# Kernel tuning notes

Hardware: AMD Instinct MI355X
Metric: run time of the kernel (lower is better)

Reference implementation:

```python
import jax, jax.numpy as jnp
import numpy as np

B, T, H, OUT, L = 125, 512, 512, 1024, 2


def _rnn_layer(xs, w_ih, w_hh, b_ih, b_hh):
    # xs: [B, T, H_in] -> scan over time with tanh recurrence
    xs_t = jnp.swapaxes(xs, 0, 1)  # [T, B, H_in]
    h0 = jnp.zeros((xs.shape[0], w_hh.shape[0]), dtype=xs.dtype)

    def step(h, x_t):
        h = jnp.tanh(x_t @ w_ih.T + b_ih + h @ w_hh.T + b_hh)
        return h, h

    h_last, hs = jax.lax.scan(step, h0, xs_t)
    return jnp.swapaxes(hs, 0, 1), h_last  # [B, T, H], [B, H]


def setup_inputs() -> dict:
    key = jax.random.key(0)
    ks = jax.random.split(key, 8)
    s = 1.0 / np.sqrt(H)
    x = jax.random.normal(ks[0], (B, T, H), dtype=jnp.float32)
    w_ih = jax.random.uniform(ks[1], (L, H, H), jnp.float32, -s, s)
    w_hh = jax.random.uniform(ks[2], (L, H, H), jnp.float32, -s, s)
    b_ih = jax.random.uniform(ks[3], (L, H), jnp.float32, -s, s)
    b_hh = jax.random.uniform(ks[4], (L, H), jnp.float32, -s, s)
    fc_w = jax.random.uniform(ks[5], (OUT, H), jnp.float32, -s, s)
    fc_b = jax.random.uniform(ks[6], (OUT,), jnp.float32, -s, s)
    return {"x": x, "w_ih": w_ih, "w_hh": w_hh, "b_ih": b_ih,
            "b_hh": b_hh, "fc_w": fc_w, "fc_b": fc_b}


def reference(x, w_ih, w_hh, b_ih, b_hh, fc_w, fc_b):
    h = x
    finals = []
    for l in range(L):  # small fixed layer loop
        h, h_last = _rnn_layer(h, w_ih[l], w_hh[l], b_ih[l], b_hh[l])
        finals.append(h_last)
    hidden = jnp.stack(finals, axis=0)  # [L, B, H]
    out = h.reshape(-1, H) @ fc_w.T + fc_b  # [B*T, OUT]
    return out, hidden
```

## Files before the change

kernel.cpp:

```cpp
#include <hip/hip_runtime.h>
#include <hip/hip_bf16.h>
#include <cstdint>

typedef short short8 __attribute__((ext_vector_type(8)));
typedef float f32x4 __attribute__((ext_vector_type(4)));
typedef uint32_t u32x2 __attribute__((ext_vector_type(2)));
typedef unsigned short u16;

#define DEVINL __device__ __forceinline__

DEVINL u16 f32_to_bf16(float f) {
  uint32_t u = __builtin_bit_cast(uint32_t, f);
  u += 0x7FFFu + ((u >> 16) & 1u);
  return (u16)(u >> 16);
}
DEVINL float bf16_to_f32(u16 b) {
  return __builtin_bit_cast(float, ((uint32_t)b) << 16);
}
DEVINL f32x4 mfma16(short8 a, short8 b, f32x4 c) {
  return __builtin_amdgcn_mfma_f32_16x16x32_bf16(a, b, c, 0, 0, 0);
}
DEVINL float tanh_e2(float x) {
  float e = __builtin_amdgcn_exp2f(x * 2.88539008177793f);
  return 1.f - __fdividef(2.f, 1.f + e);
}
DEVINL uint32_t cvt_pk_bf16(float lo, float hi) {
  uint32_t r;
  asm("v_cvt_pk_bf16_f32 %0, %1, %2" : "=v"(r) : "v"(lo), "v"(hi));
  return r;
}

__global__ void conv_bf16(const float* __restrict__ src, u16* __restrict__ dst, long n) {
  long i = ((long)blockIdx.x * blockDim.x + threadIdx.x) * 4;
  long stride = (long)gridDim.x * blockDim.x * 4;
  for (; i < n; i += stride) {
    float4 v = *(const float4*)(src + i);
    uint64_t p = (uint64_t)f32_to_bf16(v.x)
               | ((uint64_t)f32_to_bf16(v.y) << 16)
               | ((uint64_t)f32_to_bf16(v.z) << 32)
               | ((uint64_t)f32_to_bf16(v.w) << 48);
    *(uint64_t*)(dst + i) = p;
  }
}

__global__ void prep_bias(const float* __restrict__ bih, const float* __restrict__ bhh,
                          float* __restrict__ b1, float* __restrict__ b2) {
  int i = threadIdx.x;
  b1[i] = bih[i]       + bhh[i];
  b2[i] = bih[512 + i] + bhh[512 + i];
}

DEVINL void rec_window(char* LDS, int g, const u16* __restrict__ Whh,
                       const u16* __restrict__ U, u16* __restrict__ Hout,
                       float* __restrict__ hidden, u16* __restrict__ hstate, int win) {
  const int tid  = threadIdx.x;
  const int lane = tid & 63;
  const int w    = tid >> 6;
  const int q    = lane >> 4;
  const int r16  = lane & 15;
  const int t0   = win << 7;

  short8 wreg[3][16];
#pragma unroll
  for (int tt = 0; tt < 3; ++tt)
#pragma unroll
    for (int kk = 0; kk < 16; ++kk)
      wreg[tt][kk] = *(const short8*)(Whh + (size_t)(w * 64 + tt * 16 + r16) * 512 + kk * 32 + q * 8);

#pragma unroll
  for (int kk = 0; kk < 16; ++kk) {
    short8 v = *(const short8*)(Whh + (size_t)(w * 64 + 48 + r16) * 512 + kk * 32 + q * 8);
    *(short8*)(LDS + w * 16384 + kk * 1024 + q * 256 + r16 * 16) = v;
  }

  if (win == 0) {
    short8 z = {0, 0, 0, 0, 0, 0, 0, 0};
    *(short8*)(LDS + 131072 + tid * 32)      = z;
    *(short8*)(LDS + 131072 + tid * 32 + 16) = z;
  } else {
    short8 a = *(const short8*)(hstate + (size_t)g * 8192 + tid * 16);
    short8 b = *(const short8*)(hstate + (size_t)g * 8192 + tid * 16 + 8);
    *(short8*)(LDS + 131072 + tid * 32)      = a;
    *(short8*)(LDS + 131072 + tid * 32 + 16) = b;
  }

  uint32_t rd  = 131072 + q * 256 + r16 * 16;
  uint32_t wrb = 147456 + w * 2048 + (q >> 1) * 256 + r16 * 16 + (q & 1) * 8;
  const uint32_t wlb = w * 16384 + q * 256 + r16 * 16;
  const int jb = w * 64 + q * 4;
  const char* Ub = (const char*)U;
  const uint32_t ubase = (uint32_t)(g * 512 + tid) * 32;
  char* Hc = (char*)Hout;
  uint32_t hoff = (uint32_t)(g * 16 + r16) * 524288u + (uint32_t)jb * 2u + (uint32_t)t0 * 1024u;

  short8 u  = *(const short8*)(Ub + ubase + (uint32_t)t0 * 131072u);
  short8 u2 = *(const short8*)(Ub + ubase + (uint32_t)t0 * 131072u + 16);
  __syncthreads();

  for (int t = t0; t < t0 + 128; ++t) {
    f32x4 D0, D1, D2, D3;
#pragma unroll
    for (int rg = 0; rg < 4; ++rg) {
      D0[rg] = bf16_to_f32((u16)u[rg]);
      D1[rg] = bf16_to_f32((u16)u[rg + 4]);
      D2[rg] = bf16_to_f32((u16)u2[rg]);
      D3[rg] = bf16_to_f32((u16)u2[rg + 4]);
    }
    {
      uint32_t off = ubase + (uint32_t)((t + 1 <= 511) ? (t + 1) : 511) * 131072u;
      u  = *(const short8*)(Ub + off);
      u2 = *(const short8*)(Ub + off + 16);
    }
#pragma unroll
    for (int kk = 0; kk < 16; ++kk) {
      short8 hf = *(const short8*)(LDS + rd + kk * 1024);
      short8 wl = *(const short8*)(LDS + wlb + kk * 1024);
      D0 = mfma16(wreg[0][kk], hf, D0);
      D1 = mfma16(wreg[1][kk], hf, D1);
      D2 = mfma16(wreg[2][kk], hf, D2);
      D3 = mfma16(wl, hf, D3);
    }
#define EPI_TILE(Dt, tt) { \
    float e0 = tanh_e2(Dt[0]), e1 = tanh_e2(Dt[1]); \
    float e2 = tanh_e2(Dt[2]), e3 = tanh_e2(Dt[3]); \
    u32x2 pk; pk[0] = cvt_pk_bf16(e0, e1); pk[1] = cvt_pk_bf16(e2, e3); \
    *(u32x2*)(LDS + wrb + ((tt) >> 1) * 1024 + ((tt) & 1) * 512) = pk; \
    *(u32x2*)(Hc + hoff + (tt) * 32) = pk; \
  }
    EPI_TILE(D0, 0); EPI_TILE(D1, 1); EPI_TILE(D2, 2); EPI_TILE(D3, 3);
#undef EPI_TILE
    hoff += 1024;

    rd ^= 16384; wrb ^= 16384;
    asm volatile("s_waitcnt lgkmcnt(0)" ::: "memory");
    __builtin_amdgcn_s_barrier();
    asm volatile("" ::: "memory");
  }

  {
    short8 a = *(const short8*)(LDS + 131072 + tid * 32);
    short8 b = *(const short8*)(LDS + 131072 + tid * 32 + 16);
    *(short8*)(hstate + (size_t)g * 8192 + tid * 16)     = a;
    *(short8*)(hstate + (size_t)g * 8192 + tid * 16 + 8) = b;
  }

  if (win == 3) {
    int b = g * 16 + r16;
    if (b < 125) {
      uint32_t fwr = 131072 + w * 2048 + (q >> 1) * 256 + r16 * 16 + (q & 1) * 8;
#pragma unroll
      for (int tt = 0; tt < 4; ++tt) {
        u32x2 pk = *(const u32x2*)(LDS + fwr + (tt >> 1) * 1024 + (tt & 1) * 512);
        float4 v;
        v.x = __builtin_bit_cast(float, pk[0] << 16);
        v.y = __builtin_bit_cast(float, pk[0] & 0xFFFF0000u);
        v.z = __builtin_bit_cast(float, pk[1] << 16);
        v.w = __builtin_bit_cast(float, pk[1] & 0xFFFF0000u);
        *(float4*)(hidden + (size_t)b * 512 + jb + tt * 16) = v;
      }
    }
  }
}

DEVINL void gemm_tile(char* LDS, const u16* __restrict__ A, const u16* __restrict__ B,
                      const float* __restrict__ bias, void* __restrict__ out,
                      int brow, int bcol, int N, int frag) {
  u16* lA = (u16*)LDS;
  u16* lB = (u16*)(LDS + 16384);
  const int tid  = threadIdx.x;
  const int lane = tid & 63;
  const int wave = tid >> 6;
  const int wr = wave >> 2;
  const int wc = wave & 3;
  const int q   = lane >> 4;
  const int r16 = lane & 15;

  f32x4 acc[4][2];
#pragma unroll
  for (int i = 0; i < 4; ++i)
#pragma unroll
    for (int j = 0; j < 2; ++j) acc[i][j] = (f32x4){0.f, 0.f, 0.f, 0.f};

  for (int kt = 0; kt < 8; ++kt) {
#pragma unroll
    for (int s = 0; s < 2; ++s) {
      int c   = tid * 2 + s;
      int row = c >> 3;
      int cb  = (c & 7) * 16;
      int dsw = cb ^ ((row & 7) << 4);
      short8 va = *(const short8*)(A + (size_t)(brow + row) * 512 + kt * 64 + (cb >> 1));
      *(short8*)((char*)lA + row * 128 + dsw) = va;
      short8 vb = *(const short8*)(B + (size_t)(bcol + row) * 512 + kt * 64 + (cb >> 1));
      *(short8*)((char*)lB + row * 128 + dsw) = vb;
    }
    __syncthreads();
#pragma unroll
    for (int kk = 0; kk < 2; ++kk) {
      short8 af[4], bfr[2];
#pragma unroll
      for (int mt = 0; mt < 4; ++mt) {
        int row = wr * 64 + mt * 16 + r16;
        int byt = (kk * 64 + q * 16) ^ ((row & 7) << 4);
        af[mt] = *(const short8*)((const char*)lA + row * 128 + byt);
      }
#pragma unroll
      for (int nt = 0; nt < 2; ++nt) {
        int row = wc * 32 + nt * 16 + r16;
        int byt = (kk * 64 + q * 16) ^ ((row & 7) << 4);
        bfr[nt] = *(const short8*)((const char*)lB + row * 128 + byt);
      }
#pragma unroll
      for (int mt = 0; mt < 4; ++mt)
#pragma unroll
        for (int nt = 0; nt < 2; ++nt)
          acc[mt][nt] = mfma16(af[mt], bfr[nt], acc[mt][nt]);
    }
    __syncthreads();
  }

#pragma unroll
  for (int mt = 0; mt < 4; ++mt) {
#pragma unroll
    for (int nt = 0; nt < 2; ++nt) {
      int jc = bcol + wc * 32 + nt * 16 + r16;
      float bv = bias[jc];
      if (!frag) {
#pragma unroll
        for (int rg = 0; rg < 4; ++rg) {
          int mg = brow + wr * 64 + mt * 16 + q * 4 + rg;
          ((float*)out)[(size_t)mg * N + jc] = acc[mt][nt][rg] + bv;
        }
      } else {
        int tidc    = (jc >> 6) * 64 + ((jc >> 2) & 3) * 16;
        int colpart = ((jc >> 4) & 3) * 4 + (jc & 3);
#pragma unroll
        for (int rg = 0; rg < 4; ++rg) {
          int mg = brow + wr * 64 + mt * 16 + q * 4 + rg;
          int bb = mg >> 9;
          int t2 = mg & 511;
          size_t idx = (((size_t)t2 * 8 + (bb >> 4)) * 512 + tidc + (bb & 15)) * 16 + colpart;
          ((u16*)out)[idx] = f32_to_bf16(acc[mt][nt][rg] + bv);
        }
      }
    }
  }
}

__attribute__((amdgpu_flat_work_group_size(512, 512), amdgpu_waves_per_eu(2, 2)))
__global__ void phase(const u16* __restrict__ Whh1, const u16* __restrict__ Whh2,
                      u16* __restrict__ U1, u16* __restrict__ U2,
                      u16* __restrict__ H1, u16* __restrict__ H2,
                      u16* __restrict__ hs1, u16* __restrict__ hs2,
                      const u16* __restrict__ Xb, const u16* __restrict__ Wih1,
                      const u16* __restrict__ Wih2, const u16* __restrict__ FCW,
                      const float* __restrict__ b1, const float* __restrict__ b2,
                      const float* __restrict__ fcb,
                      float* __restrict__ outp, float* __restrict__ hid,
                      int rec1w, int rec2w, int njobs, int j0, int j1, int j2) {
  __shared__ char LDS[163840];
  const int bx = blockIdx.x;
  if (bx < 8) {
    if (rec1w >= 0) rec_window(LDS, bx, Whh1, U1, H1, hid, hs1, rec1w);
  } else if (bx < 16) {
    if (rec2w >= 0) rec_window(LDS, bx - 8, Whh2, U2, H2, hid + 64000, hs2, rec2w);
  } else if (njobs > 0) {
    const int widx = bx - 16;
    int jobs[3] = {j0, j1, j2};
    int cnt[3], total = 0;
    for (int i = 0; i < njobs; ++i) { cnt[i] = ((jobs[i] >> 2) == 2) ? 1000 : 500; total += cnt[i]; }
    for (int tile = widx; tile < total; tile += 240) {
      int rem = tile, jj = 0;
      while (jj < njobs - 1 && rem >= cnt[jj]) { rem -= cnt[jj]; ++jj; }
      int kind = jobs[jj] >> 2, wn = jobs[jj] & 3;
      if (kind == 0)
        gemm_tile(LDS, Xb, Wih1, b1, U1, (rem >> 2) * 512 + wn * 128, (rem & 3) * 128, 512, 1);
      else if (kind == 1)
        gemm_tile(LDS, H1, Wih2, b2, U2, (rem >> 2) * 512 + wn * 128, (rem & 3) * 128, 512, 1);
      else
        gemm_tile(LDS, H2, FCW, fcb, outp, (rem >> 3) * 512 + wn * 128, (rem & 7) * 128, 1024, 0);
    }
  }
}

#define J(k, w) ((k) * 4 + (w))

extern "C" void kernel_launch(void* const* d_in, const int* in_sizes, int n_in,
                              void* d_out, int out_size, void* d_ws, size_t ws_size,
                              hipStream_t stream) {
  const float* x   = (const float*)d_in[0];
  const float* wih = (const float*)d_in[1];
  const float* whh = (const float*)d_in[2];
  const float* bih = (const float*)d_in[3];
  const float* bhh = (const float*)d_in[4];
  const float* fcw = (const float*)d_in[5];
  const float* fcb = (const float*)d_in[6];

  char* ws = (char*)d_ws;
  float* outp = (float*)d_out;
  float* hid  = outp + 65536000;
  u16*   U1   = (u16*)d_out;

  u16* Wih1 = (u16*)(ws + 0);
  u16* Whh1 = (u16*)(ws + 524288);
  u16* Wih2 = (u16*)(ws + 1048576);
  u16* Whh2 = (u16*)(ws + 1572864);
  u16* FCW  = (u16*)(ws + 2097152);
  float* b1 = (float*)(ws + 3145728);
  float* b2 = b1 + 512;
  u16* hs1  = (u16*)(ws + 3276800);
  u16* hs2  = (u16*)(ws + 3407872);

  conv_bf16<<<2048, 256, 0, stream>>>(x, (u16*)(ws + 4194304), 32768000L);
  conv_bf16<<<256, 256, 0, stream>>>(wih,          Wih1, 262144L);
  conv_bf16<<<256, 256, 0, stream>>>(wih + 262144, Wih2, 262144L);
  conv_bf16<<<256, 256, 0, stream>>>(whh,          Whh1, 262144L);
  conv_bf16<<<256, 256, 0, stream>>>(whh + 262144, Whh2, 262144L);
  conv_bf16<<<512, 256, 0, stream>>>(fcw, FCW, 524288L);
  prep_bias<<<1, 512, 0, stream>>>(bih, bhh, b1, b2);

  u16* Xb = (u16*)(ws + 4194304);

  if (ws_size >= 205520896ull) {
    u16* U2 = (u16*)(ws + 4194304);
    u16* H1 = (u16*)(ws + 71303168);
    u16* H2 = (u16*)(ws + 138412032);
#define PH(r1, r2, nj, a, b, c) \
    phase<<<256, 512, 0, stream>>>(Whh1, Whh2, U1, U2, H1, H2, hs1, hs2, Xb, \
                                   Wih1, Wih2, FCW, b1, b2, fcb, outp, hid, \
                                   r1, r2, nj, a, b, c)
    PH(-1, -1, 1, J(0,0), 0, 0);
    PH( 0, -1, 3, J(0,1), J(0,2), J(0,3));
    PH( 1, -1, 1, J(1,0), 0, 0);
    PH( 2,  0, 1, J(1,1), 0, 0);
    PH( 3,  1, 1, J(1,2), 0, 0);
    PH(-1,  2, 2, J(1,3), J(2,0), 0);
    PH(-1,  3, 2, J(2,1), J(2,2), 0);
    PH(-1, -1, 1, J(2,3), 0, 0);
#undef PH
  } else {
    u16* U2 = U1;
    u16* H1 = (u16*)(ws + 70303744);
    u16* H2 = H1;
#define PH(r1, r2, nj, a, b, c) \
    phase<<<256, 512, 0, stream>>>(Whh1, Whh2, U1, U2, H1, H2, hs1, hs2, Xb, \
                                   Wih1, Wih2, FCW, b1, b2, fcb, outp, hid, \
                                   r1, r2, nj, a, b, c)
    PH(-1, -1, 3, J(0,0), J(0,1), J(0,2));
    PH(-1, -1, 1, J(0,3), 0, 0);
    PH( 0, -1, 0, 0, 0, 0);
    PH( 1, -1, 0, 0, 0, 0);
    PH( 2, -1, 0, 0, 0, 0);
    PH( 3, -1, 0, 0, 0, 0);
    PH(-1, -1, 3, J(1,0), J(1,1), J(1,2));
    PH(-1, -1, 1, J(1,3), 0, 0);
    PH(-1,  0, 0, 0, 0, 0);
    PH(-1,  1, 0, 0, 0, 0);
    PH(-1,  2, 0, 0, 0, 0);
    PH(-1,  3, 0, 0, 0, 0);
    PH(-1, -1, 2, J(2,0), J(2,1), 0);
    PH(-1, -1, 2, J(2,2), J(2,3), 0);
#undef PH
  }

  (void)in_sizes; (void)n_in; (void)out_size;
}
```

Before: 1.904 ms.

## Halve recurrence windows for finer overlap and fuse x conversion into GEMM

```diff
diff --git a/kernel.cpp b/kernel.cpp
--- a/kernel.cpp
+++ b/kernel.cpp
@@ -58,7 +58,7 @@
   const int w    = tid >> 6;
   const int q    = lane >> 4;
   const int r16  = lane & 15;
-  const int t0   = win << 7;
+  const int t0   = win << 6;
 
   short8 wreg[3][16];
 #pragma unroll
@@ -97,7 +97,7 @@
   short8 u2 = *(const short8*)(Ub + ubase + (uint32_t)t0 * 131072u + 16);
   __syncthreads();
 
-  for (int t = t0; t < t0 + 128; ++t) {
+  for (int t = t0; t < t0 + 64; ++t) {
     f32x4 D0, D1, D2, D3;
 #pragma unroll
     for (int rg = 0; rg < 4; ++rg) {
@@ -144,7 +144,7 @@
     *(short8*)(hstate + (size_t)g * 8192 + tid * 16 + 8) = b;
   }
 
-  if (win == 3) {
+  if (win == 7) {
     int b = g * 16 + r16;
     if (b < 125) {
       uint32_t fwr = 131072 + w * 2048 + (q >> 1) * 256 + r16 * 16 + (q & 1) * 8;
@@ -162,9 +162,10 @@
   }
 }
 
-DEVINL void gemm_tile(char* LDS, const u16* __restrict__ A, const u16* __restrict__ B,
-                      const float* __restrict__ bias, void* __restrict__ out,
-                      int brow, int bcol, int N, int frag) {
+template <int MR, int AF32, int FRAG>
+DEVINL void gemm_tile(char* LDS, const void* __restrict__ Ap,
+                      const u16* __restrict__ B, const float* __restrict__ bias,
+                      void* __restrict__ out, int brow, int bcol, int N) {
   u16* lA = (u16*)LDS;
   u16* lB = (u16*)(LDS + 16384);
   const int tid  = threadIdx.x;
@@ -174,32 +175,59 @@
   const int wc = wave & 3;
   const int q   = lane >> 4;
   const int r16 = lane & 15;
-
-  f32x4 acc[4][2];
-#pragma unroll
-  for (int i = 0; i < 4; ++i)
+  const int MT = MR / 32;
+
+  f32x4 acc[MT][2];
+#pragma unroll
+  for (int i = 0; i < MT; ++i)
 #pragma unroll
     for (int j = 0; j < 2; ++j) acc[i][j] = (f32x4){0.f, 0.f, 0.f, 0.f};
 
   for (int kt = 0; kt < 8; ++kt) {
+    if (AF32) {
+#pragma unroll
+      for (int s = 0; s < 2; ++s) {
+        int c   = tid * 2 + s;
+        int row = c >> 3;
+        int seg = c & 7;
+        const float* src = (const float*)Ap + (size_t)(brow + row) * 512 + kt * 64 + seg * 8;
+        float4 a0 = *(const float4*)(src);
+        float4 a1 = *(const float4*)(src + 4);
+        u32x2 p0, p1;
+        p0[0] = cvt_pk_bf16(a0.x, a0.y); p0[1] = cvt_pk_bf16(a0.z, a0.w);
+        p1[0] = cvt_pk_bf16(a1.x, a1.y); p1[1] = cvt_pk_bf16(a1.z, a1.w);
+        int dsw = (seg * 16) ^ ((row & 7) << 4);
+        *(u32x2*)((char*)lA + row * 128 + dsw)     = p0;
+        *(u32x2*)((char*)lA + row * 128 + (dsw ^ 8)) = p1;
+      }
+    } else {
+      const int CH = MR / 64;
+#pragma unroll
+      for (int s = 0; s < CH; ++s) {
+        int c   = tid * CH + s;
+        int row = c >> 3;
+        int cb  = (c & 7) * 16;
+        int dsw = cb ^ ((row & 7) << 4);
+        short8 va = *(const short8*)((const u16*)Ap + (size_t)(brow + row) * 512 + kt * 64 + (cb >> 1));
+        *(short8*)((char*)lA + row * 128 + dsw) = va;
+      }
+    }
 #pragma unroll
     for (int s = 0; s < 2; ++s) {
       int c   = tid * 2 + s;
       int row = c >> 3;
       int cb  = (c & 7) * 16;
       int dsw = cb ^ ((row & 7) << 4);
-      short8 va = *(const short8*)(A + (size_t)(brow + row) * 512 + kt * 64 + (cb >> 1));
-      *(short8*)((char*)lA + row * 128 + dsw) = va;
       short8 vb = *(const short8*)(B + (size_t)(bcol + row) * 512 + kt * 64 + (cb >> 1));
       *(short8*)((char*)lB + row * 128 + dsw) = vb;
     }
     __syncthreads();
 #pragma unroll
     for (int kk = 0; kk < 2; ++kk) {
-      short8 af[4], bfr[2];
-#pragma unroll
-      for (int mt = 0; mt < 4; ++mt) {
-        int row = wr * 64 + mt * 16 + r16;
+      short8 af[MT], bfr[2];
+#pragma unroll
+      for (int mt = 0; mt < MT; ++mt) {
+        int row = wr * (MR / 2) + mt * 16 + r16;
         int byt = (kk * 64 + q * 16) ^ ((row & 7) << 4);
         af[mt] = *(const short8*)((const char*)lA + row * 128 + byt);
       }
@@ -210,7 +238,7 @@
         bfr[nt] = *(const short8*)((const char*)lB + row * 128 + byt);
       }
 #pragma unroll
-      for (int mt = 0; mt < 4; ++mt)
+      for (int mt = 0; mt < MT; ++mt)
 #pragma unroll
         for (int nt = 0; nt < 2; ++nt)
           acc[mt][nt] = mfma16(af[mt], bfr[nt], acc[mt][nt]);
@@ -219,15 +247,15 @@
   }
 
 #pragma unroll
-  for (int mt = 0; mt < 4; ++mt) {
+  for (int mt = 0; mt < MT; ++mt) {
 #pragma unroll
     for (int nt = 0; nt < 2; ++nt) {
       int jc = bcol + wc * 32 + nt * 16 + r16;
       float bv = bias[jc];
-      if (!frag) {
+      if (!FRAG) {
 #pragma unroll
         for (int rg = 0; rg < 4; ++rg) {
-          int mg = brow + wr * 64 + mt * 16 + q * 4 + rg;
+          int mg = brow + wr * (MR / 2) + mt * 16 + q * 4 + rg;
           ((float*)out)[(size_t)mg * N + jc] = acc[mt][nt][rg] + bv;
         }
       } else {
@@ -235,7 +263,7 @@
         int colpart = ((jc >> 4) & 3) * 4 + (jc & 3);
 #pragma unroll
         for (int rg = 0; rg < 4; ++rg) {
-          int mg = brow + wr * 64 + mt * 16 + q * 4 + rg;
+          int mg = brow + wr * (MR / 2) + mt * 16 + q * 4 + rg;
           int bb = mg >> 9;
           int t2 = mg & 511;
           size_t idx = (((size_t)t2 * 8 + (bb >> 4)) * 512 + tidc + (bb & 15)) * 16 + colpart;
@@ -251,12 +279,12 @@
                       u16* __restrict__ U1, u16* __restrict__ U2,
                       u16* __restrict__ H1, u16* __restrict__ H2,
                       u16* __restrict__ hs1, u16* __restrict__ hs2,
-                      const u16* __restrict__ Xb, const u16* __restrict__ Wih1,
+                      const float* __restrict__ Xf, const u16* __restrict__ Wih1,
                       const u16* __restrict__ Wih2, const u16* __restrict__ FCW,
                       const float* __restrict__ b1, const float* __restrict__ b2,
                       const float* __restrict__ fcb,
                       float* __restrict__ outp, float* __restrict__ hid,
-                      int rec1w, int rec2w, int njobs, int j0, int j1, int j2) {
+                      int rec1w, int rec2w, int njobs, int j0, int j1, int j2, int j3) {
   __shared__ char LDS[163840];
   const int bx = blockIdx.x;
   if (bx < 8) {
@@ -265,24 +293,27 @@
     if (rec2w >= 0) rec_window(LDS, bx - 8, Whh2, U2, H2, hid + 64000, hs2, rec2w);
   } else if (njobs > 0) {
     const int widx = bx - 16;
-    int jobs[3] = {j0, j1, j2};
-    int cnt[3], total = 0;
-    for (int i = 0; i < njobs; ++i) { cnt[i] = ((jobs[i] >> 2) == 2) ? 1000 : 500; total += cnt[i]; }
+    int jobs[4] = {j0, j1, j2, j3};
+    int cnt[4], total = 0;
+    for (int i = 0; i < njobs; ++i) { cnt[i] = ((jobs[i] >> 4) == 2) ? 1000 : 500; total += cnt[i]; }
     for (int tile = widx; tile < total; tile += 240) {
       int rem = tile, jj = 0;
       while (jj < njobs - 1 && rem >= cnt[jj]) { rem -= cnt[jj]; ++jj; }
-      int kind = jobs[jj] >> 2, wn = jobs[jj] & 3;
+      int kind = jobs[jj] >> 4, wn = jobs[jj] & 15;
       if (kind == 0)
-        gemm_tile(LDS, Xb, Wih1, b1, U1, (rem >> 2) * 512 + wn * 128, (rem & 3) * 128, 512, 1);
+        gemm_tile<128, 1, 1>(LDS, Xf, Wih1, b1, U1,
+                             (rem >> 2) * 512 + wn * 128, (rem & 3) * 128, 512);
       else if (kind == 1)
-        gemm_tile(LDS, H1, Wih2, b2, U2, (rem >> 2) * 512 + wn * 128, (rem & 3) * 128, 512, 1);
+        gemm_tile<64, 0, 1>(LDS, H1, Wih2, b2, U2,
+                            (rem >> 2) * 512 + wn * 64, (rem & 3) * 128, 512);
       else
-        gemm_tile(LDS, H2, FCW, fcb, outp, (rem >> 3) * 512 + wn * 128, (rem & 7) * 128, 1024, 0);
-    }
-  }
-}
-
-#define J(k, w) ((k) * 4 + (w))
+        gemm_tile<128, 0, 0>(LDS, H2, FCW, fcb, outp,
+                             (rem >> 3) * 512 + wn * 128, (rem & 7) * 128, 1024);
+    }
+  }
+}
+
+#define J(k, w) ((k) * 16 + (w))
 
 extern "C" void kernel_launch(void* const* d_in, const int* in_sizes, int n_in,
                               void* d_out, int out_size, void* d_ws, size_t ws_size,
@@ -310,7 +341,6 @@
   u16* hs1  = (u16*)(ws + 3276800);
   u16* hs2  = (u16*)(ws + 3407872);
 
-  conv_bf16<<<2048, 256, 0, stream>>>(x, (u16*)(ws + 4194304), 32768000L);
   conv_bf16<<<256, 256, 0, stream>>>(wih,          Wih1, 262144L);
   conv_bf16<<<256, 256, 0, stream>>>(wih + 262144, Wih2, 262144L);
   conv_bf16<<<256, 256, 0, stream>>>(whh,          Whh1, 262144L);
@@ -318,47 +348,42 @@
   conv_bf16<<<512, 256, 0, stream>>>(fcw, FCW, 524288L);
   prep_bias<<<1, 512, 0, stream>>>(bih, bhh, b1, b2);
 
-  u16* Xb = (u16*)(ws + 4194304);
-
   if (ws_size >= 205520896ull) {
     u16* U2 = (u16*)(ws + 4194304);
     u16* H1 = (u16*)(ws + 71303168);
     u16* H2 = (u16*)(ws + 138412032);
-#define PH(r1, r2, nj, a, b, c) \
-    phase<<<256, 512, 0, stream>>>(Whh1, Whh2, U1, U2, H1, H2, hs1, hs2, Xb, \
+#define PH(r1, r2, nj, a, b, c, d) \
+    phase<<<256, 512, 0, stream>>>(Whh1, Whh2, U1, U2, H1, H2, hs1, hs2, x, \
                                    Wih1, Wih2, FCW, b1, b2, fcb, outp, hid, \
-                                   r1, r2, nj, a, b, c)
-    PH(-1, -1, 1, J(0,0), 0, 0);
-    PH( 0, -1, 3, J(0,1), J(0,2), J(0,3));
-    PH( 1, -1, 1, J(1,0), 0, 0);
-    PH( 2,  0, 1, J(1,1), 0, 0);
-    PH( 3,  1, 1, J(1,2), 0, 0);
-    PH(-1,  2, 2, J(1,3), J(2,0), 0);
-    PH(-1,  3, 2, J(2,1), J(2,2), 0);
-    PH(-1, -1, 1, J(2,3), 0, 0);
+                                   r1, r2, nj, a, b, c, d)
+    PH(-1, -1, 1, J(0,0), 0, 0, 0);
+    PH( 0, -1, 3, J(0,1), J(0,2), J(0,3), 0);
+    PH( 1, -1, 1, J(1,0), 0, 0, 0);
+    PH( 2,  0, 1, J(1,1), 0, 0, 0);
+    PH( 3,  1, 1, J(1,2), 0, 0, 0);
+    PH( 4,  2, 1, J(1,3), 0, 0, 0);
+    PH( 5,  3, 1, J(1,4), 0, 0, 0);
+    PH( 6,  4, 1, J(1,5), 0, 0, 0);
+    PH( 7,  5, 1, J(1,6), 0, 0, 0);
+    PH(-1,  6, 3, J(1,7), J(2,0), J(2,1), 0);
+    PH(-1,  7, 1, J(2,2), 0, 0, 0);
+    PH(-1, -1, 1, J(2,3), 0, 0, 0);
 #undef PH
   } else {
     u16* U2 = U1;
-    u16* H1 = (u16*)(ws + 70303744);
+    u16* H1 = (u16*)(ws + 4194304);
     u16* H2 = H1;
-#define PH(r1, r2, nj, a, b, c) \
-    phase<<<256, 512, 0, stream>>>(Whh1, Whh2, U1, U2, H1, H2, hs1, hs2, Xb, \
+#define PH(r1, r2, nj, a, b, c, d) \
+    phase<<<256, 512, 0, stream>>>(Whh1, Whh2, U1, U2, H1, H2, hs1, hs2, x, \
                                    Wih1, Wih2, FCW, b1, b2, fcb, outp, hid, \
-                                   r1, r2, nj, a, b, c)
-    PH(-1, -1, 3, J(0,0), J(0,1), J(0,2));
-    PH(-1, -1, 1, J(0,3), 0, 0);
-    PH( 0, -1, 0, 0, 0, 0);
-    PH( 1, -1, 0, 0, 0, 0);
-    PH( 2, -1, 0, 0, 0, 0);
-    PH( 3, -1, 0, 0, 0, 0);
-    PH(-1, -1, 3, J(1,0), J(1,1), J(1,2));
-    PH(-1, -1, 1, J(1,3), 0, 0);
-    PH(-1,  0, 0, 0, 0, 0);
-    PH(-1,  1, 0, 0, 0, 0);
-    PH(-1,  2, 0, 0, 0, 0);
-    PH(-1,  3, 0, 0, 0, 0);
-    PH(-1, -1, 2, J(2,0), J(2,1), 0);
-    PH(-1, -1, 2, J(2,2), J(2,3), 0);
+                                   r1, r2, nj, a, b, c, d)
+    PH(-1, -1, 4, J(0,0), J(0,1), J(0,2), J(0,3));
+    for (int w = 0; w < 8; ++w) PH(w, -1, 0, 0, 0, 0, 0);
+    PH(-1, -1, 4, J(1,0), J(1,1), J(1,2), J(1,3));
+    PH(-1, -1, 4, J(1,4), J(1,5), J(1,6), J(1,7));
+    for (int w = 0; w < 8; ++w) PH(-1, w, 0, 0, 0, 0, 0);
+    PH(-1, -1, 2, J(2,0), J(2,1), 0, 0);
+    PH(-1, -1, 2, J(2,2), J(2,3), 0, 0);
 #undef PH
   }
 
```

Result: faster. 1.720 ms (-9.7%).
